# Kernel tuning notes

Measured on AMD Instinct MI355X. Metric: run time of the kernel, lower is better.

## Reference

```python
import jax, jax.numpy as jnp
import numpy as np


def setup_inputs() -> dict:
    key = jax.random.key(0)
    k1, k2 = jax.random.split(key)
    B, N, F, K = 8, 8192, 128, 512
    x = jax.random.normal(k1, (B, N, F), dtype=jnp.float32)
    cluster_centers = jax.random.normal(k2, (K, F), dtype=jnp.float32)
    return {"x": x, "cluster_centers": cluster_centers}


def reference(x, cluster_centers):
    # same math as sqrt(sum((x - c)^2)) without the [B,N,K,F] intermediate).
    x_sq = jnp.sum(x * x, axis=-1, keepdims=True)                 # [B, N, 1]
    c_sq = jnp.sum(cluster_centers * cluster_centers, axis=-1)    # [K]
    cross = jnp.einsum("bnf,kf->bnk", x, cluster_centers)         # [B, N, K]
    d2 = jnp.maximum(x_sq + c_sq[None, None, :] - 2.0 * cross, 0.0)
    distances = jnp.sqrt(d2)                                      # [B, N, K]
    associations = jax.nn.softmax(-distances, axis=-1)            # [B, N, K]
    output = jnp.einsum("bnk,kf->bnf", associations, cluster_centers)
    return output
```

## Files before the change

kernel.cpp:

```cpp
#include <hip/hip_runtime.h>
#include <hip/hip_bf16.h>

typedef short v8s __attribute__((ext_vector_type(8)));
typedef float v16f __attribute__((ext_vector_type(16)));
typedef unsigned v2u __attribute__((ext_vector_type(2)));

#define F_ 128
#define K_ 512
#define M_ 65536
#define CH_SH 17408
#define CB_OFF 9216

typedef __attribute__((address_space(1))) const char gch;
typedef __attribute__((address_space(3))) char lch;

__device__ __forceinline__ short f2bf(float f) {
    union { float f; unsigned u; } v; v.f = f;
    unsigned u = v.u;
    u = (u + 0x7FFFu + ((u >> 16) & 1u)) >> 16;
    return (short)u;
}
__device__ __forceinline__ float bf2f(short s) {
    union { float f; unsigned u; } v;
    v.u = ((unsigned)(unsigned short)s) << 16;
    return v.f;
}

#if __has_builtin(__builtin_amdgcn_permlane32_swap)
#define HAVE_PLS 1
#endif

__device__ __forceinline__ void pswap(unsigned &a, unsigned &b, int lane) {
#ifdef HAVE_PLS
    v2u r = __builtin_amdgcn_permlane32_swap(a, b, false, false);
    a = (unsigned)r.x; b = (unsigned)r.y;
#else
    unsigned sa = (unsigned)__shfl_xor((int)a, 32);
    unsigned sb = (unsigned)__shfl_xor((int)b, 32);
    if (lane & 32) a = sb; else b = sa;
#endif
}

__global__ void prep_kernel(const float* __restrict__ centers, short* __restrict__ G) {
    const int c = blockIdx.x;
    const int f = threadIdx.x;
    const int ch = c >> 6, c64 = c & 63;
    const size_t base = (size_t)ch * CH_SH;
    float v = centers[c * F_ + f];
    short b = f2bf(v);
    float vb = bf2f(b);
    { const int ks = f >> 4, h = (f >> 3) & 1, j = f & 7;
      G[base + (size_t)((ks * 2 + h) * 64 + c64) * 8 + j] = b; }
    { const int kap = c64 >> 4, hh = (c64 >> 3) & 1, jj = c64 & 7;
      G[base + CB_OFF + (size_t)((kap * 2 + hh) * F_ + f) * 8 + jj] = b; }
    float s = vb * vb;
    #pragma unroll
    for (int off = 1; off < 64; off <<= 1) s += __shfl_xor(s, off);
    __shared__ float part[2];
    if ((f & 63) == 0) part[f >> 6] = s;
    __syncthreads();
    if (f < 16) {
        const float csq = part[0] + part[1];
        const float chv = -0.5f * csq;
        const short vh = f2bf(chv);
        const short vl = f2bf(chv - bf2f(vh));
        const short val = (f == 0) ? vh : (f == 1) ? vl : (f == 2) ? (short)0x3F80 : (short)0;
        const int h2 = f >> 3, j2 = f & 7;
        G[base + (size_t)((16 + h2) * 64 + c64) * 8 + j2] = val;
    }
}

__device__ __forceinline__ void stage_chunk(const short* __restrict__ G, short* dst,
                                            int ch, int wave, int lane) {
    const char* src = (const char*)(G + (size_t)ch * CH_SH);
    lch* d = (lch*)dst;
    #pragma unroll
    for (int t = 0; t < 4; ++t) {
        const int g = t * 512 + wave * 64 + lane;
        __builtin_amdgcn_global_load_lds((gch*)(src + (size_t)g * 16),
                                         d + (size_t)(t * 512 + wave * 64) * 16, 16, 0, 0);
    }
    if (wave < 2) {
        const int g = 2048 + wave * 64 + lane;
        __builtin_amdgcn_global_load_lds((gch*)(src + (size_t)g * 16),
                                         d + (size_t)(2048 + wave * 64) * 16, 16, 0, 0);
    }
}

__global__ __launch_bounds__(512, 2) void cluster_kernel(
        const float* __restrict__ x, const short* __restrict__ G,
        float* __restrict__ out) {
    __shared__ __align__(16) short SB[3][CH_SH];
    const int tid = threadIdx.x;
    const int wave = tid >> 6, lane = tid & 63;
    const int h = lane >> 5, c32 = lane & 31;
    const int row0 = blockIdx.x * 256 + wave * 32;

    const float4* xr4 = (const float4*)(x + (size_t)(row0 + c32) * F_);
    float4 xl[16];
    #pragma unroll
    for (int ks = 0; ks < 8; ++ks) {
        xl[2 * ks]     = xr4[ks * 4 + h * 2];
        xl[2 * ks + 1] = xr4[ks * 4 + h * 2 + 1];
    }
    v8s Bx[9];
    float xs = 0.f;
    #pragma unroll
    for (int ks = 0; ks < 8; ++ks) {
        float vv[8] = {xl[2*ks].x, xl[2*ks].y, xl[2*ks].z, xl[2*ks].w,
                       xl[2*ks+1].x, xl[2*ks+1].y, xl[2*ks+1].z, xl[2*ks+1].w};
        v8s fr;
        #pragma unroll
        for (int j = 0; j < 8; ++j) {
            short bb = f2bf(vv[j]);
            fr[j] = bb;
            float r = bf2f(bb);
            xs += r * r;
        }
        Bx[ks] = fr;
    }
    xs += __shfl_xor(xs, 32);
    {
        const float xh = -0.5f * xs;
        const short sxh = f2bf(xh);
        const short sxl = f2bf(xh - bf2f(sxh));
        v8s e = (v8s){0, 0, 0, 0, 0, 0, 0, 0};
        if (h == 0) { e[0] = (short)0x3F80; e[1] = (short)0x3F80; e[2] = sxh; e[3] = sxl; }
        Bx[8] = e;
    }

    v16f Of[4];
    #pragma unroll
    for (int ft = 0; ft < 4; ++ft)
        #pragma unroll
        for (int e2 = 0; e2 < 16; ++e2) Of[ft][e2] = 0.f;
    float lden = 0.f;

    short* const SB0 = &SB[0][0];
    const int off = blockIdx.x & 7;
    stage_chunk(G, SB0, off, wave, lane);
    stage_chunk(G, SB0 + CH_SH, (off + 1) & 7, wave, lane);

    #pragma unroll 1
    for (int j = 0; j < 8; ++j) {
        __syncthreads();
        if (j < 6)
            stage_chunk(G, SB0 + (size_t)((j + 2) % 3) * CH_SH, (off + j + 2) & 7, wave, lane);
        const short* CbS = SB0 + (size_t)(j % 3) * CH_SH;
        const short* CTS = CbS + CB_OFF;

        v16f a0, a1;
        #pragma unroll
        for (int e2 = 0; e2 < 16; ++e2) { a0[e2] = 0.f; a1[e2] = 0.f; }
        {
            v8s f0a = *(const v8s*)&CbS[(size_t)((0 * 2 + h) * 64 + c32) * 8];
            v8s f1a = *(const v8s*)&CbS[(size_t)((0 * 2 + h) * 64 + 32 + c32) * 8];
            v8s f0b = *(const v8s*)&CbS[(size_t)((1 * 2 + h) * 64 + c32) * 8];
            v8s f1b = *(const v8s*)&CbS[(size_t)((1 * 2 + h) * 64 + 32 + c32) * 8];
            #pragma unroll
            for (int ks = 0; ks < 9; ++ks) {
                v8s c0 = f0a, c1 = f1a;
                f0a = f0b; f1a = f1b;
                if (ks < 7) {
                    f0b = *(const v8s*)&CbS[(size_t)(((ks + 2) * 2 + h) * 64 + c32) * 8];
                    f1b = *(const v8s*)&CbS[(size_t)(((ks + 2) * 2 + h) * 64 + 32 + c32) * 8];
                }
                a0 = __builtin_amdgcn_mfma_f32_32x32x16_bf16(c0, Bx[ks], a0, 0, 0, 0);
                a1 = __builtin_amdgcn_mfma_f32_32x32x16_bf16(c1, Bx[ks], a1, 0, 0, 0);
            }
        }

        #pragma unroll
        for (int ct = 0; ct < 2; ++ct) {
            v8s cf[8];
            #pragma unroll
            for (int kp = 0; kp < 2; ++kp)
                #pragma unroll
                for (int ft = 0; ft < 4; ++ft)
                    cf[kp * 4 + ft] = *(const v8s*)
                        &CTS[(size_t)(((ct * 2 + kp) * 2 + h) * F_ + ft * 32 + c32) * 8];
            const v16f acc = ct ? a1 : a0;
            unsigned U[8];
            #pragma unroll
            for (int t = 0; t < 8; ++t) {
                const float d20 = fmaxf(-2.0f * acc[2 * t], 0.f);
                const float d21 = fmaxf(-2.0f * acc[2 * t + 1], 0.f);
                const float p0 = __expf(-__builtin_amdgcn_sqrtf(d20));
                const float p1 = __expf(-__builtin_amdgcn_sqrtf(d21));
                union { __hip_bfloat162 hh; unsigned u; } cv;
                cv.hh = __float22bfloat162_rn(make_float2(p0, p1));
                U[t] = cv.u;
                lden += __uint_as_float(cv.u << 16);
                lden += __uint_as_float(cv.u & 0xffff0000u);
            }
            #pragma unroll
            for (int kp = 0; kp < 2; ++kp) {
                unsigned s0 = U[4 * kp],     s2 = U[4 * kp + 2];
                unsigned s1 = U[4 * kp + 1], s3 = U[4 * kp + 3];
                pswap(s0, s2, lane);
                pswap(s1, s3, lane);
                union { v8s v; unsigned u[4]; } pf;
                pf.u[0] = s0; pf.u[1] = s1; pf.u[2] = s2; pf.u[3] = s3;
                #pragma unroll
                for (int ft = 0; ft < 4; ++ft)
                    Of[ft] = __builtin_amdgcn_mfma_f32_32x32x16_bf16(pf.v, cf[kp * 4 + ft], Of[ft], 0, 0, 0);
            }
        }
    }

    lden += __shfl_xor(lden, 32);
    const float inv = 1.0f / lden;
    float invr[16];
    #pragma unroll
    for (int r = 0; r < 16; ++r)
        invr[r] = __shfl(inv, (r & 3) + 8 * (r >> 2) + 4 * h);
    #pragma unroll
    for (int ft = 0; ft < 4; ++ft)
        #pragma unroll
        for (int r = 0; r < 16; ++r) {
            const int xrow = (r & 3) + 8 * (r >> 2) + 4 * h;
            out[(size_t)(row0 + xrow) * F_ + ft * 32 + c32] = Of[ft][r] * invr[r];
        }
}

extern "C" void kernel_launch(void* const* d_in, const int* in_sizes, int n_in,
                              void* d_out, int out_size, void* d_ws, size_t ws_size,
                              hipStream_t stream) {
    const float* x       = (const float*)d_in[0];
    const float* centers = (const float*)d_in[1];
    float* out = (float*)d_out;
    short* G = (short*)d_ws;
    prep_kernel<<<K_, F_, 0, stream>>>(centers, G);
    cluster_kernel<<<M_ / 256, 512, 0, stream>>>(x, G, out);
}
```

Baseline: 105.0 us.

## Load transposed centers from global into registers, shrink LDS staging to double buffer

Only the first-GEMM center fragments (Cb) are now staged in LDS, double-buffered instead of triple-buffered whole chunks. The transposed center fragments (CT) for the second GEMM are loaded straight from global memory into 16 registers per lane at the top of each iteration. The first staging is also issued before the x loads. This cuts LDS use per block and LDS read traffic, but adds global/L2 loads with latency exposed inside the loop and more register pressure at 2 blocks per CU.

Result: no change. 106.4 us (+1.3%).

```diff
diff --git a/kernel.cpp b/kernel.cpp
--- a/kernel.cpp
+++ b/kernel.cpp
@@ -10,6 +10,7 @@
 #define M_ 65536
 #define CH_SH 17408
 #define CB_OFF 9216
+#define CB_SH 9216
 
 typedef __attribute__((address_space(1))) const char gch;
 typedef __attribute__((address_space(3))) char lch;
@@ -70,31 +71,85 @@
     }
 }
 
-__device__ __forceinline__ void stage_chunk(const short* __restrict__ G, short* dst,
-                                            int ch, int wave, int lane) {
+__device__ __forceinline__ void stage_cb(const short* __restrict__ G, short* dst,
+                                         int ch, int wave, int lane) {
     const char* src = (const char*)(G + (size_t)ch * CH_SH);
     lch* d = (lch*)dst;
     #pragma unroll
-    for (int t = 0; t < 4; ++t) {
+    for (int t = 0; t < 2; ++t) {
         const int g = t * 512 + wave * 64 + lane;
         __builtin_amdgcn_global_load_lds((gch*)(src + (size_t)g * 16),
                                          d + (size_t)(t * 512 + wave * 64) * 16, 16, 0, 0);
     }
     if (wave < 2) {
-        const int g = 2048 + wave * 64 + lane;
+        const int g = 1024 + wave * 64 + lane;
         __builtin_amdgcn_global_load_lds((gch*)(src + (size_t)g * 16),
-                                         d + (size_t)(2048 + wave * 64) * 16, 16, 0, 0);
+                                         d + (size_t)(1024 + wave * 64) * 16, 16, 0, 0);
+    }
+}
+
+__device__ __forceinline__ void stage1(const short* CbS, const v8s* Bx,
+                                       v16f& a0, v16f& a1, int h, int c32) {
+    #pragma unroll
+    for (int e2 = 0; e2 < 16; ++e2) { a0[e2] = 0.f; a1[e2] = 0.f; }
+    v8s f0a = *(const v8s*)&CbS[(size_t)((0 * 2 + h) * 64 + c32) * 8];
+    v8s f1a = *(const v8s*)&CbS[(size_t)((0 * 2 + h) * 64 + 32 + c32) * 8];
+    v8s f0b = *(const v8s*)&CbS[(size_t)((1 * 2 + h) * 64 + c32) * 8];
+    v8s f1b = *(const v8s*)&CbS[(size_t)((1 * 2 + h) * 64 + 32 + c32) * 8];
+    #pragma unroll
+    for (int ks = 0; ks < 9; ++ks) {
+        v8s c0 = f0a, c1 = f1a;
+        f0a = f0b; f1a = f1b;
+        if (ks < 7) {
+            f0b = *(const v8s*)&CbS[(size_t)(((ks + 2) * 2 + h) * 64 + c32) * 8];
+            f1b = *(const v8s*)&CbS[(size_t)(((ks + 2) * 2 + h) * 64 + 32 + c32) * 8];
+        }
+        a0 = __builtin_amdgcn_mfma_f32_32x32x16_bf16(c0, Bx[ks], a0, 0, 0, 0);
+        a1 = __builtin_amdgcn_mfma_f32_32x32x16_bf16(c1, Bx[ks], a1, 0, 0, 0);
+    }
+}
+
+__device__ __forceinline__ void epi_ct(const v16f acc, const v8s* cf,
+                                       float& lden, v16f (&Of)[4], int c32, int lane) {
+    unsigned U[8];
+    #pragma unroll
+    for (int t = 0; t < 8; ++t) {
+        const float d20 = fmaxf(-2.0f * acc[2 * t], 0.f);
+        const float d21 = fmaxf(-2.0f * acc[2 * t + 1], 0.f);
+        const float p0 = __expf(-__builtin_amdgcn_sqrtf(d20));
+        const float p1 = __expf(-__builtin_amdgcn_sqrtf(d21));
+        union { __hip_bfloat162 hh; unsigned u; } cv;
+        cv.hh = __float22bfloat162_rn(make_float2(p0, p1));
+        U[t] = cv.u;
+        lden += __uint_as_float(cv.u << 16);
+        lden += __uint_as_float(cv.u & 0xffff0000u);
+    }
+    #pragma unroll
+    for (int kp = 0; kp < 2; ++kp) {
+        unsigned s0 = U[4 * kp],     s2 = U[4 * kp + 2];
+        unsigned s1 = U[4 * kp + 1], s3 = U[4 * kp + 3];
+        pswap(s0, s2, lane);
+        pswap(s1, s3, lane);
+        union { v8s v; unsigned u[4]; } pf;
+        pf.u[0] = s0; pf.u[1] = s1; pf.u[2] = s2; pf.u[3] = s3;
+        #pragma unroll
+        for (int ft = 0; ft < 4; ++ft)
+            Of[ft] = __builtin_amdgcn_mfma_f32_32x32x16_bf16(pf.v, cf[kp * 4 + ft], Of[ft], 0, 0, 0);
     }
 }
 
 __global__ __launch_bounds__(512, 2) void cluster_kernel(
         const float* __restrict__ x, const short* __restrict__ G,
         float* __restrict__ out) {
-    __shared__ __align__(16) short SB[3][CH_SH];
+    __shared__ __align__(16) short SB[2][CB_SH];
     const int tid = threadIdx.x;
     const int wave = tid >> 6, lane = tid & 63;
     const int h = lane >> 5, c32 = lane & 31;
     const int row0 = blockIdx.x * 256 + wave * 32;
+
+    short* const SB0 = &SB[0][0];
+    const int off = blockIdx.x & 7;
+    stage_cb(G, SB0, off, wave, lane);
 
     const float4* xr4 = (const float4*)(x + (size_t)(row0 + c32) * F_);
     float4 xl[16];
@@ -136,76 +191,30 @@
         for (int e2 = 0; e2 < 16; ++e2) Of[ft][e2] = 0.f;
     float lden = 0.f;
 
-    short* const SB0 = &SB[0][0];
-    const int off = blockIdx.x & 7;
-    stage_chunk(G, SB0, off, wave, lane);
-    stage_chunk(G, SB0 + CH_SH, (off + 1) & 7, wave, lane);
-
     #pragma unroll 1
     for (int j = 0; j < 8; ++j) {
         __syncthreads();
-        if (j < 6)
-            stage_chunk(G, SB0 + (size_t)((j + 2) % 3) * CH_SH, (off + j + 2) & 7, wave, lane);
-        const short* CbS = SB0 + (size_t)(j % 3) * CH_SH;
-        const short* CTS = CbS + CB_OFF;
-
-        v16f a0, a1;
-        #pragma unroll
-        for (int e2 = 0; e2 < 16; ++e2) { a0[e2] = 0.f; a1[e2] = 0.f; }
-        {
-            v8s f0a = *(const v8s*)&CbS[(size_t)((0 * 2 + h) * 64 + c32) * 8];
-            v8s f1a = *(const v8s*)&CbS[(size_t)((0 * 2 + h) * 64 + 32 + c32) * 8];
-            v8s f0b = *(const v8s*)&CbS[(size_t)((1 * 2 + h) * 64 + c32) * 8];
-            v8s f1b = *(const v8s*)&CbS[(size_t)((1 * 2 + h) * 64 + 32 + c32) * 8];
-            #pragma unroll
-            for (int ks = 0; ks < 9; ++ks) {
-                v8s c0 = f0a, c1 = f1a;
-                f0a = f0b; f1a = f1b;
-                if (ks < 7) {
-                    f0b = *(const v8s*)&CbS[(size_t)(((ks + 2) * 2 + h) * 64 + c32) * 8];
-                    f1b = *(const v8s*)&CbS[(size_t)(((ks + 2) * 2 + h) * 64 + 32 + c32) * 8];
-                }
-                a0 = __builtin_amdgcn_mfma_f32_32x32x16_bf16(c0, Bx[ks], a0, 0, 0, 0);
-                a1 = __builtin_amdgcn_mfma_f32_32x32x16_bf16(c1, Bx[ks], a1, 0, 0, 0);
-            }
-        }
-
-        #pragma unroll
-        for (int ct = 0; ct < 2; ++ct) {
-            v8s cf[8];
+
+        const int ch = (off + j) & 7;
+        const short* CTg = G + (size_t)ch * CH_SH + CB_OFF;
+        v8s cf[16];
+        #pragma unroll
+        for (int ct = 0; ct < 2; ++ct)
             #pragma unroll
             for (int kp = 0; kp < 2; ++kp)
                 #pragma unroll
                 for (int ft = 0; ft < 4; ++ft)
-                    cf[kp * 4 + ft] = *(const v8s*)
-                        &CTS[(size_t)(((ct * 2 + kp) * 2 + h) * F_ + ft * 32 + c32) * 8];
-            const v16f acc = ct ? a1 : a0;
-            unsigned U[8];
-            #pragma unroll
-            for (int t = 0; t < 8; ++t) {
-                const float d20 = fmaxf(-2.0f * acc[2 * t], 0.f);
-                const float d21 = fmaxf(-2.0f * acc[2 * t + 1], 0.f);
-                const float p0 = __expf(-__builtin_amdgcn_sqrtf(d20));
-                const float p1 = __expf(-__builtin_amdgcn_sqrtf(d21));
-                union { __hip_bfloat162 hh; unsigned u; } cv;
-                cv.hh = __float22bfloat162_rn(make_float2(p0, p1));
-                U[t] = cv.u;
-                lden += __uint_as_float(cv.u << 16);
-                lden += __uint_as_float(cv.u & 0xffff0000u);
-            }
-            #pragma unroll
-            for (int kp = 0; kp < 2; ++kp) {
-                unsigned s0 = U[4 * kp],     s2 = U[4 * kp + 2];
-                unsigned s1 = U[4 * kp + 1], s3 = U[4 * kp + 3];
-                pswap(s0, s2, lane);
-                pswap(s1, s3, lane);
-                union { v8s v; unsigned u[4]; } pf;
-                pf.u[0] = s0; pf.u[1] = s1; pf.u[2] = s2; pf.u[3] = s3;
-                #pragma unroll
-                for (int ft = 0; ft < 4; ++ft)
-                    Of[ft] = __builtin_amdgcn_mfma_f32_32x32x16_bf16(pf.v, cf[kp * 4 + ft], Of[ft], 0, 0, 0);
-            }
-        }
+                    cf[ct * 8 + kp * 4 + ft] = *(const v8s*)
+                        &CTg[(size_t)(((ct * 2 + kp) * 2 + h) * F_ + ft * 32 + c32) * 8];
+
+        if (j < 7)
+            stage_cb(G, SB0 + (size_t)((j + 1) & 1) * CB_SH, (off + j + 1) & 7, wave, lane);
+
+        const short* CbS = SB0 + (size_t)(j & 1) * CB_SH;
+        v16f a0, a1;
+        stage1(CbS, Bx, a0, a1, h, c32);
+        epi_ct(a0, cf,     lden, Of, c32, lane);
+        epi_ct(a1, cf + 8, lden, Of, c32, lane);
     }
 
     lden += __shfl_xor(lden, 32);
```
